# Kernel optimization log

Measured on AMD Instinct MI355X. Metric: run time of the kernel, lower is better.

Reference implementation:

```python
import jax, jax.numpy as jnp
import numpy as np

NC = 2_000_000   # clauses
NV = 500_000     # variables
E = 6_000_000    # edges per polarity


def _inv_sqrt_deg(deg):
    # deg^-0.5 with inf (deg==0) replaced by 0, nan-safe for autodiff
    safe = jnp.where(deg > 0, deg, 1.0)
    return jnp.where(deg > 0, safe ** -0.5, 0.0)


def _conv(x_src, x_trg, inv_src, inv_trg, src, trg, n_trg):
    # G4GCNConv: message = norm * x_j + x_i, aggr='add'
    # (lin_src+relu in the original is dead code: propagate uses raw x)
    norm = inv_src[src] * inv_trg[trg]                     # [E]
    msg = norm[:, None] * x_src[src] + x_trg[trg]          # [E, 2]
    return jax.ops.segment_sum(msg, trg, num_segments=n_trg)  # [n_trg, 2]


def setup_inputs() -> dict:
    key = jax.random.key(0)
    ks = jax.random.split(key, 16)
    inp = {
        'x_clause': jax.random.normal(ks[0], (NC, 1), jnp.float32),
        'x_variable': jax.random.normal(ks[1], (NV, 1), jnp.float32),
        'deg_clause': jax.random.randint(ks[2], (NC,), 0, 16).astype(jnp.float32),
        'deg_variable': jax.random.randint(ks[3], (NV,), 0, 48).astype(jnp.float32),
        'pos_src': jax.random.randint(ks[4], (E,), 0, NC, jnp.int32),
        'pos_trg': jax.random.randint(ks[5], (E,), 0, NV, jnp.int32),
        'neg_src': jax.random.randint(ks[6], (E,), 0, NC, jnp.int32),
        'neg_trg': jax.random.randint(ks[7], (E,), 0, NV, jnp.int32),
        'W0c': jax.random.normal(ks[8], (1, 2), jnp.float32),
        'b0c': jax.random.normal(ks[9], (2,), jnp.float32) * 0.1,
        'W0v': jax.random.normal(ks[10], (1, 2), jnp.float32),
        'b0v': jax.random.normal(ks[11], (2,), jnp.float32) * 0.1,
        'Wc': jax.random.normal(ks[12], (4, 6, 2), jnp.float32) * 0.4,
        'bc': jax.random.normal(ks[13], (4, 2), jnp.float32) * 0.1,
        'Wv': jax.random.normal(ks[14], (4, 6, 2), jnp.float32) * 0.4,
        'bv': jax.random.normal(ks[15], (4, 2), jnp.float32) * 0.1,
    }
    return inp


def reference(x_clause, x_variable, deg_clause, deg_variable,
              pos_src, pos_trg, neg_src, neg_trg,
              W0c, b0c, W0v, b0v, Wc, bc, Wv, bv):
    nc, nv = x_clause.shape[0], x_variable.shape[0]
    inv_c = _inv_sqrt_deg(deg_clause)
    inv_v = _inv_sqrt_deg(deg_variable)

    xc = x_clause @ W0c + b0c    # [NC, 2]
    xv = x_variable @ W0v + b0v  # [NV, 2]

    for l in range(4):
        prev_c, prev_v = xc, xv
        # target 'variable': clause -> variable edges (pos, then neg)
        v_pos = _conv(xc, xv, inv_c, inv_v, pos_src, pos_trg, nv)
        v_neg = _conv(xc, xv, inv_c, inv_v, neg_src, neg_trg, nv)
        # target 'clause': reversed edges, variable -> clause
        c_pos = _conv(xv, xc, inv_v, inv_c, pos_trg, pos_src, nc)
        c_neg = _conv(xv, xc, inv_v, inv_c, neg_trg, neg_src, nc)
        # HeteroConv aggr='cat' then cat with previous state, then 6->2 Linear
        xv = jnp.concatenate([v_pos, v_neg, prev_v], axis=1) @ Wv[l] + bv[l]
        xc = jnp.concatenate([c_pos, c_neg, prev_c], axis=1) @ Wc[l] + bc[l]

    return xv  # [NV, 2]
```

## Files before the change

kernel.cpp:

```cpp
#include <hip/hip_runtime.h>


#define GAB 256
#define BB  1024
#define CAPE 26624

static inline int cdiv_h(long long a, long long b) { return (int)((a + b - 1) / b); }

__device__ inline float bf_lo(unsigned u) { return __uint_as_float(u << 16); }
__device__ inline float bf_hi(unsigned u) { return __uint_as_float(u & 0xffff0000u); }
__device__ inline unsigned packy(float a, float b) {
    unsigned ua = __float_as_uint(a), ub = __float_as_uint(b);
    ua = (ua + 0x7fffu + ((ua >> 16) & 1u)) >> 16;
    ub = (ub + 0x7fffu + ((ub >> 16) & 1u)) & 0xffff0000u;
    return ua | ub;
}


__global__ __launch_bounds__(BB) void hist_both(
    const int* __restrict__ keyV, const int* __restrict__ keyC,
    int e, int chunk, int sv, int sc, int nbv, int nbc,
    unsigned* __restrict__ histV, unsigned* __restrict__ histC) {
    extern __shared__ unsigned h[];
    unsigned* hv = h;
    unsigned* hc = h + nbv * 4;
    int blk = blockIdx.x, tid = threadIdx.x;
    for (int i = tid; i < (nbv + nbc) * 4; i += blockDim.x) h[i] = 0u;
    __syncthreads();
    int s = blk * chunk, epos = min(e, s + chunk);
    int r = tid & 3;
    for (int i = s + tid; i < epos; i += blockDim.x) {
        atomicAdd(&hv[(((unsigned)(keyV[i] >> sv)) << 2) | r], 1u);
        atomicAdd(&hc[(((unsigned)(keyC[i] >> sc)) << 2) | r], 1u);
    }
    __syncthreads();
    for (int i = tid; i < nbv; i += blockDim.x)
        histV[(size_t)i * GAB + blk] = hv[4 * i] + hv[4 * i + 1] + hv[4 * i + 2] + hv[4 * i + 3];
    for (int i = tid; i < nbc; i += blockDim.x)
        histC[(size_t)i * GAB + blk] = hc[4 * i] + hc[4 * i + 1] + hc[4 * i + 2] + hc[4 * i + 3];
}

__global__ void rowscan256(const unsigned* __restrict__ hist, unsigned* __restrict__ rowscan,
                           unsigned* __restrict__ row_total) {
    __shared__ unsigned ts[256];
    int b = blockIdx.x, t = threadIdx.x;
    unsigned v0 = hist[(size_t)b * GAB + t];
    ts[t] = v0;
    __syncthreads();
    for (int off = 1; off < 256; off <<= 1) {
        unsigned v = (t >= off) ? ts[t - off] : 0u;
        __syncthreads();
        ts[t] += v;
        __syncthreads();
    }
    rowscan[(size_t)b * GAB + t] = ts[t] - v0;
    if (t == 255) row_total[b] = ts[255];
}

__global__ void basescan2(const unsigned* __restrict__ totP, const unsigned* __restrict__ totN,
                          unsigned* __restrict__ base, unsigned* __restrict__ baseNeg, int nb) {
    __shared__ unsigned a[2048];
    __shared__ unsigned ts[1024];
    int t = threadIdx.x;
    a[t] = (t < nb) ? (totP[t] + totN[t]) : 0u;
    a[t + 1024] = (t + 1024 < nb) ? (totP[t + 1024] + totN[t + 1024]) : 0u;
    __syncthreads();
    unsigned a0 = a[2 * t], a1 = a[2 * t + 1];
    unsigned sum = a0 + a1;
    ts[t] = sum;
    __syncthreads();
    for (int off = 1; off < 1024; off <<= 1) {
        unsigned v = (t >= off) ? ts[t - off] : 0u;
        __syncthreads();
        ts[t] += v;
        __syncthreads();
    }
    unsigned b0 = ts[t] - sum;
    if (2 * t <= nb) base[2 * t] = b0;
    if (2 * t + 1 <= nb) base[2 * t + 1] = b0 + a0;
    if (2 * t < nb) baseNeg[2 * t] = b0 + totP[2 * t];
    if (2 * t + 1 < nb) baseNeg[2 * t + 1] = b0 + a0 + totP[2 * t + 1];
}

__global__ __launch_bounds__(BB) void scatter_sb(
    const int* __restrict__ key, const int* __restrict__ pay,
    int e, int chunk, int kshift, int nb,
    const unsigned* __restrict__ rowscan, const unsigned* __restrict__ base,
    unsigned* __restrict__ out) {
    extern __shared__ unsigned cur[];
    int blk = blockIdx.x, tid = threadIdx.x;
    for (int i = tid; i < nb; i += blockDim.x)
        cur[i] = base[i] + rowscan[(size_t)i * GAB + blk];
    __syncthreads();
    int s = blk * chunk, epos = min(e, s + chunk);
    unsigned mask = (1u << kshift) - 1u;
    for (int i = s + tid; i < epos; i += blockDim.x) {
        int k = key[i];
        int b = k >> kshift;
        unsigned p = atomicAdd(&cur[b], 1u);
        out[p] = ((unsigned)pay[i] << kshift) | ((unsigned)k & mask);
    }
}

__global__ __launch_bounds__(1024) void localsort_v_m(
    const unsigned* __restrict__ ent, const unsigned* __restrict__ base,
    const unsigned* __restrict__ baseNeg, int nsb, int nv, int cs,
    unsigned* __restrict__ srcs, unsigned* __restrict__ rp, unsigned* __restrict__ cnts) {
    __shared__ unsigned h[4096];
    __shared__ unsigned ts[1024];
    __shared__ unsigned buf[CAPE];
    int s = blockIdx.x, t = threadIdx.x;
    unsigned sb = base[s], pe = baseNeg[s], se = base[s + 1];
    bool fits = (se - sb) <= (unsigned)CAPE;
    for (int k = 0; k < 4; ++k) h[t * 4 + k] = 0u;
    __syncthreads();
    for (unsigned i = sb + t; i < pe; i += 1024) {
        unsigned u = ent[i];
        atomicAdd(&h[((u & 1023u) << 2) | ((u >> 10) >> cs)], 1u);
    }
    __syncthreads();
    unsigned pc[4];
    for (int k = 0; k < 4; ++k) pc[k] = h[t * 4 + k];
    __syncthreads();
    for (unsigned i = pe + t; i < se; i += 1024) {
        unsigned u = ent[i];
        atomicAdd(&h[((u & 1023u) << 2) | ((u >> 10) >> cs)], 1u);
    }
    __syncthreads();
    unsigned v0[4];
    unsigned sum = 0;
    for (int k = 0; k < 4; ++k) { v0[k] = h[t * 4 + k]; sum += v0[k]; }
    ts[t] = sum;
    __syncthreads();
    for (int off = 1; off < 1024; off <<= 1) {
        unsigned x = (t >= off) ? ts[t - off] : 0u;
        __syncthreads();
        ts[t] += x;
        __syncthreads();
    }
    unsigned ex = ts[t] - sum;
    unsigned hx[4];
    for (int k = 0; k < 4; ++k) { hx[k] = ex; ex += v0[k]; }
    int node = s * 1024 + t;
    if (node < nv) {
        for (int ch = 0; ch < 4; ++ch) rp[(size_t)node * 4 + ch] = sb + hx[ch];
        unsigned cp = pc[0] + pc[1] + pc[2] + pc[3];
        unsigned tot = v0[0] + v0[1] + v0[2] + v0[3];
        cnts[node] = (cp << 16) | (tot - cp);
    }
    if (s == nsb - 1 && t == 0) rp[(size_t)nv * 4] = se;
    for (int k = 0; k < 4; ++k) h[t * 4 + k] = hx[k];
    __syncthreads();
    if (fits) {
        for (unsigned i = sb + t; i < pe; i += 1024) {
            unsigned u = ent[i];
            unsigned p = atomicAdd(&h[((u & 1023u) << 2) | ((u >> 10) >> cs)], 1u);
            buf[p] = u >> 10;
        }
        for (unsigned i = pe + t; i < se; i += 1024) {
            unsigned u = ent[i];
            unsigned p = atomicAdd(&h[((u & 1023u) << 2) | ((u >> 10) >> cs)], 1u);
            buf[p] = 0x80000000u | (u >> 10);
        }
        __syncthreads();
        unsigned n = se - sb;
        for (unsigned i = t; i < n; i += 1024) srcs[sb + i] = buf[i];
    } else {
        for (unsigned i = sb + t; i < pe; i += 1024) {
            unsigned u = ent[i];
            unsigned p = atomicAdd(&h[((u & 1023u) << 2) | ((u >> 10) >> cs)], 1u);
            srcs[sb + p] = u >> 10;
        }
        for (unsigned i = pe + t; i < se; i += 1024) {
            unsigned u = ent[i];
            unsigned p = atomicAdd(&h[((u & 1023u) << 2) | ((u >> 10) >> cs)], 1u);
            srcs[sb + p] = 0x80000000u | (u >> 10);
        }
    }
}

__global__ __launch_bounds__(1024) void localsort_c_m(
    const unsigned* __restrict__ ent, const unsigned* __restrict__ base,
    const unsigned* __restrict__ baseNeg, int nsb, int nc,
    unsigned* __restrict__ srcs, unsigned* __restrict__ rp, unsigned* __restrict__ cnts) {
    __shared__ unsigned h[4096];
    __shared__ unsigned ts[1024];
    __shared__ unsigned buf[CAPE];
    int s = blockIdx.x, t = threadIdx.x;
    unsigned sb = base[s], pe = baseNeg[s], se = base[s + 1];
    bool fits = (se - sb) <= (unsigned)CAPE;
    for (int k = 0; k < 4; ++k) h[t * 4 + k] = 0u;
    __syncthreads();
    for (unsigned i = sb + t; i < pe; i += 1024)
        atomicAdd(&h[ent[i] & 4095u], 1u);
    __syncthreads();
    unsigned pc[4];
    for (int k = 0; k < 4; ++k) pc[k] = h[t * 4 + k];
    __syncthreads();
    for (unsigned i = pe + t; i < se; i += 1024)
        atomicAdd(&h[ent[i] & 4095u], 1u);
    __syncthreads();
    unsigned v0[4];
    unsigned sum = 0;
    for (int k = 0; k < 4; ++k) { v0[k] = h[t * 4 + k]; sum += v0[k]; }
    ts[t] = sum;
    __syncthreads();
    for (int off = 1; off < 1024; off <<= 1) {
        unsigned x = (t >= off) ? ts[t - off] : 0u;
        __syncthreads();
        ts[t] += x;
        __syncthreads();
    }
    unsigned ex = ts[t] - sum;
    unsigned hx[4];
    for (int k = 0; k < 4; ++k) { hx[k] = ex; ex += v0[k]; }
    int node0 = s * 4096 + t * 4;
    for (int k = 0; k < 4; ++k) {
        int node = node0 + k;
        if (node < nc) {
            rp[node] = sb + hx[k];
            cnts[node] = (pc[k] << 16) | (v0[k] - pc[k]);
        }
    }
    if (s == nsb - 1 && t == 0) rp[nc] = se;
    for (int k = 0; k < 4; ++k) h[t * 4 + k] = hx[k];
    __syncthreads();
    if (fits) {
        for (unsigned i = sb + t; i < pe; i += 1024) {
            unsigned u = ent[i];
            unsigned p = atomicAdd(&h[u & 4095u], 1u);
            buf[p] = u >> 12;
        }
        for (unsigned i = pe + t; i < se; i += 1024) {
            unsigned u = ent[i];
            unsigned p = atomicAdd(&h[u & 4095u], 1u);
            buf[p] = 0x80000000u | (u >> 12);
        }
        __syncthreads();
        unsigned n = se - sb;
        for (unsigned i = t; i < n; i += 1024) srcs[sb + i] = buf[i];
    } else {
        for (unsigned i = sb + t; i < pe; i += 1024) {
            unsigned u = ent[i];
            unsigned p = atomicAdd(&h[u & 4095u], 1u);
            srcs[sb + p] = u >> 12;
        }
        for (unsigned i = pe + t; i < se; i += 1024) {
            unsigned u = ent[i];
            unsigned p = atomicAdd(&h[u & 4095u], 1u);
            srcs[sb + p] = 0x80000000u | (u >> 12);
        }
    }
}


__global__ void init_c_kernel(const float* __restrict__ x, const float* __restrict__ deg,
                              const float* __restrict__ W0, const float* __restrict__ b0,
                              float2* __restrict__ xc, unsigned* __restrict__ yc, int n) {
    int i = blockIdx.x * blockDim.x + threadIdx.x;
    if (i >= n) return;
    float xi = x[i];
    float2 o = make_float2(fmaf(xi, W0[0], b0[0]), fmaf(xi, W0[1], b0[1]));
    xc[i] = o;
    float d = deg[i];
    float inv = (d > 0.f) ? rsqrtf(d) : 0.f;
    yc[i] = packy(inv * o.x, inv * o.y);
}

__global__ void init_v_kernel(const float* __restrict__ x, const float* __restrict__ deg,
                              const float* __restrict__ W0, const float* __restrict__ b0,
                              float2* __restrict__ xv, unsigned* __restrict__ yv, int n) {
    int i = blockIdx.x * blockDim.x + threadIdx.x;
    if (i >= n) return;
    float xi = x[i];
    float2 o = make_float2(fmaf(xi, W0[0], b0[0]), fmaf(xi, W0[1], b0[1]));
    xv[i] = o;
    float d = deg[i];
    float inv = (d > 0.f) ? rsqrtf(d) : 0.f;
    yv[i] = packy(inv * o.x, inv * o.y);
}


__global__ __launch_bounds__(256) void v_chunk_q(
    const unsigned* __restrict__ rp, const unsigned* __restrict__ srcs,
    const unsigned* __restrict__ yc, float4* __restrict__ acc, int nv, int k) {
    int gt = blockIdx.x * blockDim.x + threadIdx.x;
    int i = gt >> 2, q = gt & 3;
    if (i >= nv) return;
    unsigned s0 = rp[(size_t)i * 4 + k], e0 = rp[(size_t)i * 4 + k + 1];
    float ax = 0.f, ay = 0.f, bx = 0.f, by = 0.f;
    for (unsigned j = s0 + q; j < e0; j += 4) {
        unsigned u = srcs[j];
        unsigned yw = yc[u & 0x7fffffffu];
        float lo = bf_lo(yw), hi = bf_hi(yw);
        float tp = (u & 0x80000000u) ? 0.f : 1.f;
        ax = fmaf(tp, lo, ax); ay = fmaf(tp, hi, ay);
        bx = fmaf(1.f - tp, lo, bx); by = fmaf(1.f - tp, hi, by);
    }
    for (int m = 1; m < 4; m <<= 1) {
        ax += __shfl_xor(ax, m, 4);
        ay += __shfl_xor(ay, m, 4);
        bx += __shfl_xor(bx, m, 4);
        by += __shfl_xor(by, m, 4);
    }
    if (q == 0) {
        float4 a = (k == 0) ? make_float4(0.f, 0.f, 0.f, 0.f) : acc[i];
        a.x += ax; a.y += ay; a.z += bx; a.w += by;
        acc[i] = a;
    }
}

__global__ __launch_bounds__(256) void v_chunk_last(
    const unsigned* __restrict__ rp, const unsigned* __restrict__ srcs,
    const unsigned* __restrict__ yc, const float4* __restrict__ acc,
    const unsigned* __restrict__ cnts, float2* __restrict__ xv,
    const float* __restrict__ deg_v, const float* __restrict__ W,
    const float* __restrict__ bias, unsigned* __restrict__ yv_out, int nv, int writeY) {
    int gt = blockIdx.x * blockDim.x + threadIdx.x;
    int i = gt >> 2, q = gt & 3;
    if (i >= nv) return;
    unsigned s0 = rp[(size_t)i * 4 + 3], e0 = rp[(size_t)i * 4 + 4];
    float ax = 0.f, ay = 0.f, bx = 0.f, by = 0.f;
    for (unsigned j = s0 + q; j < e0; j += 4) {
        unsigned u = srcs[j];
        unsigned yw = yc[u & 0x7fffffffu];
        float lo = bf_lo(yw), hi = bf_hi(yw);
        float tp = (u & 0x80000000u) ? 0.f : 1.f;
        ax = fmaf(tp, lo, ax); ay = fmaf(tp, hi, ay);
        bx = fmaf(1.f - tp, lo, bx); by = fmaf(1.f - tp, hi, by);
    }
    for (int m = 1; m < 4; m <<= 1) {
        ax += __shfl_xor(ax, m, 4);
        ay += __shfl_xor(ay, m, 4);
        bx += __shfl_xor(bx, m, 4);
        by += __shfl_xor(by, m, 4);
    }
    if (q == 0) {
        float4 a = acc[i];
        a.x += ax; a.y += ay; a.z += bx; a.w += by;
        unsigned ct = cnts[i];
        float cp = (float)(ct >> 16), cn = (float)(ct & 0xffffu);
        float2 xi = xv[i];
        float dv = deg_v[i];
        float iv = (dv > 0.f) ? rsqrtf(dv) : 0.f;
        float m0 = fmaf(iv, a.x, cp * xi.x);
        float m1 = fmaf(iv, a.y, cp * xi.y);
        float m2 = fmaf(iv, a.z, cn * xi.x);
        float m3 = fmaf(iv, a.w, cn * xi.y);
        float o0 = bias[0] + m0 * W[0] + m1 * W[2] + m2 * W[4] + m3 * W[6] + xi.x * W[8] + xi.y * W[10];
        float o1 = bias[1] + m0 * W[1] + m1 * W[3] + m2 * W[5] + m3 * W[7] + xi.x * W[9] + xi.y * W[11];
        xv[i] = make_float2(o0, o1);
        if (writeY) yv_out[i] = packy(iv * o0, iv * o1);
    }
}

__global__ __launch_bounds__(256) void c_layer_m(
    const unsigned* __restrict__ rp, const unsigned* __restrict__ srcs,
    const unsigned* __restrict__ cnts, const unsigned* __restrict__ yv,
    float2* __restrict__ xc, const float* __restrict__ deg_c,
    unsigned* __restrict__ yc, const float* __restrict__ W,
    const float* __restrict__ bias, int nc, int writeX) {
    int gt = blockIdx.x * blockDim.x + threadIdx.x;
    int i = gt >> 2, q = gt & 3;
    if (i >= nc) return;
    unsigned s0 = rp[i], e0 = rp[i + 1];
    float ax = 0.f, ay = 0.f, bx = 0.f, by = 0.f;
    for (unsigned j = s0 + q; j < e0; j += 4) {
        unsigned u = srcs[j];
        unsigned yw = yv[u & 0x7fffffffu];
        float lo = bf_lo(yw), hi = bf_hi(yw);
        float tp = (u & 0x80000000u) ? 0.f : 1.f;
        ax = fmaf(tp, lo, ax); ay = fmaf(tp, hi, ay);
        bx = fmaf(1.f - tp, lo, bx); by = fmaf(1.f - tp, hi, by);
    }
    for (int m = 1; m < 4; m <<= 1) {
        ax += __shfl_xor(ax, m, 4);
        ay += __shfl_xor(ay, m, 4);
        bx += __shfl_xor(bx, m, 4);
        by += __shfl_xor(by, m, 4);
    }
    if (q == 0) {
        unsigned ct = cnts[i];
        float cp = (float)(ct >> 16), cn = (float)(ct & 0xffffu);
        float2 xi = xc[i];
        float dc = deg_c[i];
        float ic = (dc > 0.f) ? rsqrtf(dc) : 0.f;
        float m0 = fmaf(ic, ax, cp * xi.x);
        float m1 = fmaf(ic, ay, cp * xi.y);
        float m2 = fmaf(ic, bx, cn * xi.x);
        float m3 = fmaf(ic, by, cn * xi.y);
        float o0 = bias[0] + m0 * W[0] + m1 * W[2] + m2 * W[4] + m3 * W[6] + xi.x * W[8] + xi.y * W[10];
        float o1 = bias[1] + m0 * W[1] + m1 * W[3] + m2 * W[5] + m3 * W[7] + xi.x * W[9] + xi.y * W[11];
        if (writeX) xc[i] = make_float2(o0, o1);
        yc[i] = packy(ic * o0, ic * o1);
    }
}


__global__ void init_nodes(const float* __restrict__ x, const float* __restrict__ deg,
                           const float* __restrict__ W0, const float* __restrict__ b0,
                           float2* __restrict__ xf, float* __restrict__ inv, int n) {
    int i = blockIdx.x * blockDim.x + threadIdx.x;
    if (i >= n) return;
    float xi = x[i];
    xf[i] = make_float2(fmaf(xi, W0[0], b0[0]), fmaf(xi, W0[1], b0[1]));
    float d = deg[i];
    inv[i] = (d > 0.0f) ? (1.0f / sqrtf(d)) : 0.0f;
}

__global__ void count_edges(const int* __restrict__ src, const int* __restrict__ trg,
                            float* __restrict__ cnt_src, float* __restrict__ cnt_trg, int e) {
    int i = blockIdx.x * blockDim.x + threadIdx.x;
    if (i >= e) return;
    atomicAdd(&cnt_src[src[i]], 1.0f);
    atomicAdd(&cnt_trg[trg[i]], 1.0f);
}

__global__ void edge_pass(const int* __restrict__ src, const int* __restrict__ trg,
                          const float2* __restrict__ xc, const float2* __restrict__ xv,
                          const float* __restrict__ inv_c, const float* __restrict__ inv_v,
                          float2* __restrict__ Sv, float2* __restrict__ Sc, int e) {
    int i = blockIdx.x * blockDim.x + threadIdx.x;
    if (i >= e) return;
    int c = src[i];
    int v = trg[i];
    float ic = inv_c[c], iv = inv_v[v];
    float2 a = xc[c];
    float2 b = xv[v];
    atomicAdd(&Sv[v].x, a.x * ic);
    atomicAdd(&Sv[v].y, a.y * ic);
    atomicAdd(&Sc[c].x, b.x * iv);
    atomicAdd(&Sc[c].y, b.y * iv);
}

__global__ void node_update(float2* __restrict__ x, const float2* __restrict__ Sp,
                            const float2* __restrict__ Sn, const float* __restrict__ inv,
                            const float* __restrict__ cp, const float* __restrict__ cn,
                            const float* __restrict__ W, const float* __restrict__ b, int n) {
    int i = blockIdx.x * blockDim.x + threadIdx.x;
    if (i >= n) return;
    float2 xi = x[i];
    float ii = inv[i];
    float2 sp = Sp[i], sn = Sn[i];
    float cpi = cp[i], cni = cn[i];
    float m0 = fmaf(ii, sp.x, cpi * xi.x);
    float m1 = fmaf(ii, sp.y, cpi * xi.y);
    float m2 = fmaf(ii, sn.x, cni * xi.x);
    float m3 = fmaf(ii, sn.y, cni * xi.y);
    float o0 = b[0] + m0 * W[0] + m1 * W[2] + m2 * W[4] + m3 * W[6] + xi.x * W[8] + xi.y * W[10];
    float o1 = b[1] + m0 * W[1] + m1 * W[3] + m2 * W[5] + m3 * W[7] + xi.x * W[9] + xi.y * W[11];
    x[i] = make_float2(o0, o1);
}


extern "C" void kernel_launch(void* const* d_in, const int* in_sizes, int n_in,
                              void* d_out, int out_size, void* d_ws, size_t ws_size,
                              hipStream_t stream) {
    const float* x_clause   = (const float*)d_in[0];
    const float* x_variable = (const float*)d_in[1];
    const float* deg_clause = (const float*)d_in[2];
    const float* deg_var    = (const float*)d_in[3];
    const int*   pos_src    = (const int*)d_in[4];
    const int*   pos_trg    = (const int*)d_in[5];
    const int*   neg_src    = (const int*)d_in[6];
    const int*   neg_trg    = (const int*)d_in[7];
    const float* W0c        = (const float*)d_in[8];
    const float* b0c        = (const float*)d_in[9];
    const float* W0v        = (const float*)d_in[10];
    const float* b0v        = (const float*)d_in[11];
    const float* Wc         = (const float*)d_in[12];
    const float* bc         = (const float*)d_in[13];
    const float* Wv         = (const float*)d_in[14];
    const float* bv         = (const float*)d_in[15];

    const int nc = in_sizes[0];
    const int nv = in_sizes[1];
    const int e  = in_sizes[4];
    const int B = 256;

    const int NSBV = cdiv_h(nv, 1024);
    const int NSBC = cdiv_h(nc, 4096);
    const int maxnb = NSBV > NSBC ? NSBV : NSBC;
    const bool pack_ok = (nc <= (1 << 21)) && (nv <= (1 << 19)) &&
                         (NSBV <= 2040) && (NSBC <= 2040);

    int cs = 0;
    while ((4LL << cs) < nc) cs++;

    {
        size_t off = 0;
        auto alloc = [&](size_t bytes) {
            void* p = (char*)d_ws + off;
            off += (bytes + 255) & ~(size_t)255;
            return p;
        };
        unsigned* srcs_v = (unsigned*)alloc((size_t)2 * e * 4);
        unsigned* srcs_c = (unsigned*)alloc((size_t)2 * e * 4);
        unsigned* rp_v   = (unsigned*)alloc((size_t)4 * (nv + 1) * 4);
        unsigned* rp_c   = (unsigned*)alloc((size_t)(nc + 1) * 4);
        unsigned* cnts_v = (unsigned*)alloc((size_t)nv * 4);
        unsigned* cnts_c = (unsigned*)alloc((size_t)nc * 4);
        const size_t overlay = off;
        unsigned* temp    = (unsigned*)alloc((size_t)2 * e * 4);
        unsigned* histVP  = (unsigned*)alloc((size_t)maxnb * GAB * 4);
        unsigned* histVN  = (unsigned*)alloc((size_t)maxnb * GAB * 4);
        unsigned* histCP  = (unsigned*)alloc((size_t)maxnb * GAB * 4);
        unsigned* histCN  = (unsigned*)alloc((size_t)maxnb * GAB * 4);
        unsigned* rsVP    = (unsigned*)alloc((size_t)maxnb * GAB * 4);
        unsigned* rsVN    = (unsigned*)alloc((size_t)maxnb * GAB * 4);
        unsigned* rsCP    = (unsigned*)alloc((size_t)maxnb * GAB * 4);
        unsigned* rsCN    = (unsigned*)alloc((size_t)maxnb * GAB * 4);
        unsigned* totVP   = (unsigned*)alloc((size_t)maxnb * 4);
        unsigned* totVN   = (unsigned*)alloc((size_t)maxnb * 4);
        unsigned* totCP   = (unsigned*)alloc((size_t)maxnb * 4);
        unsigned* totCN   = (unsigned*)alloc((size_t)maxnb * 4);
        unsigned* baseV   = (unsigned*)alloc((size_t)(NSBV + 1) * 4);
        unsigned* baseVN  = (unsigned*)alloc((size_t)(NSBV + 1) * 4);
        unsigned* baseC   = (unsigned*)alloc((size_t)(NSBC + 1) * 4);
        unsigned* baseCN  = (unsigned*)alloc((size_t)(NSBC + 1) * 4);
        const size_t build_end = off;
        off = overlay;
        float4*   accv    = (float4*)alloc((size_t)nv * 16);
        float2*   xc      = (float2*)alloc((size_t)nc * 8);
        unsigned* yc      = (unsigned*)alloc((size_t)nc * 4);
        unsigned* yvA     = (unsigned*)alloc((size_t)nv * 4);
        unsigned* yvB     = (unsigned*)alloc((size_t)nv * 4);
        const size_t layer_end = off;
        const size_t required = build_end > layer_end ? build_end : layer_end;

        if (required <= ws_size && pack_ok) {
            const int chunk = cdiv_h(e, GAB);
            hist_both<<<GAB, BB, (size_t)(NSBV + NSBC) * 16, stream>>>(
                pos_trg, pos_src, e, chunk, 10, 12, NSBV, NSBC, histVP, histCP);
            hist_both<<<GAB, BB, (size_t)(NSBV + NSBC) * 16, stream>>>(
                neg_trg, neg_src, e, chunk, 10, 12, NSBV, NSBC, histVN, histCN);
            rowscan256<<<NSBV, B, 0, stream>>>(histVP, rsVP, totVP);
            rowscan256<<<NSBV, B, 0, stream>>>(histVN, rsVN, totVN);
            rowscan256<<<NSBC, B, 0, stream>>>(histCP, rsCP, totCP);
            rowscan256<<<NSBC, B, 0, stream>>>(histCN, rsCN, totCN);
            basescan2<<<1, 1024, 0, stream>>>(totVP, totVN, baseV, baseVN, NSBV);
            basescan2<<<1, 1024, 0, stream>>>(totCP, totCN, baseC, baseCN, NSBC);
            scatter_sb<<<GAB, BB, (size_t)NSBV * 4, stream>>>(pos_trg, pos_src, e, chunk,
                                                              10, NSBV, rsVP, baseV, temp);
            scatter_sb<<<GAB, BB, (size_t)NSBV * 4, stream>>>(neg_trg, neg_src, e, chunk,
                                                              10, NSBV, rsVN, baseVN, temp);
            localsort_v_m<<<NSBV, 1024, 0, stream>>>(temp, baseV, baseVN, NSBV, nv, cs,
                                                     srcs_v, rp_v, cnts_v);
            scatter_sb<<<GAB, BB, (size_t)NSBC * 4, stream>>>(pos_src, pos_trg, e, chunk,
                                                              12, NSBC, rsCP, baseC, temp);
            scatter_sb<<<GAB, BB, (size_t)NSBC * 4, stream>>>(neg_src, neg_trg, e, chunk,
                                                              12, NSBC, rsCN, baseCN, temp);
            localsort_c_m<<<NSBC, 1024, 0, stream>>>(temp, baseC, baseCN, NSBC, nc,
                                                     srcs_c, rp_c, cnts_c);

            float2* xv = (float2*)d_out;
            init_c_kernel<<<cdiv_h(nc, B), B, 0, stream>>>(x_clause, deg_clause, W0c, b0c, xc, yc, nc);
            init_v_kernel<<<cdiv_h(nv, B), B, 0, stream>>>(x_variable, deg_var, W0v, b0v, xv, yvA, nv);

            unsigned* ycur = yvA;
            unsigned* ynxt = yvB;
            for (int l = 0; l < 4; ++l) {
                for (int k = 0; k < 3; ++k) {
                    v_chunk_q<<<cdiv_h((long long)nv * 4, B), B, 0, stream>>>(
                        rp_v, srcs_v, yc, accv, nv, k);
                }
                v_chunk_last<<<cdiv_h((long long)nv * 4, B), B, 0, stream>>>(
                    rp_v, srcs_v, yc, accv, cnts_v, xv, deg_var,
                    Wv + l * 12, bv + l * 2, ynxt, nv, (l < 2) ? 1 : 0);
                if (l < 3) {
                    c_layer_m<<<cdiv_h((long long)nc * 4, B), B, 0, stream>>>(
                        rp_c, srcs_c, cnts_c, ycur, xc, deg_clause, yc,
                        Wc + l * 12, bc + l * 2, nc, (l < 2) ? 1 : 0);
                }
                unsigned* ty = ycur; ycur = ynxt; ynxt = ty;
            }
            return;
        }
    }

    char* p = (char*)d_ws;
    float2* Sv_pos = (float2*)p; p += (size_t)nv * sizeof(float2);
    float2* Sv_neg = (float2*)p; p += (size_t)nv * sizeof(float2);
    float2* Sc_pos = (float2*)p; p += (size_t)nc * sizeof(float2);
    float2* Sc_neg = (float2*)p; p += (size_t)nc * sizeof(float2);
    const size_t s_bytes = (size_t)(2 * nv + 2 * nc) * sizeof(float2);
    float2* xc2 = (float2*)p; p += (size_t)nc * sizeof(float2);
    float* inv_c = (float*)p; p += (size_t)nc * sizeof(float);
    float* inv_v = (float*)p; p += (size_t)nv * sizeof(float);
    float* cntc_pos = (float*)p; p += (size_t)nc * sizeof(float);
    float* cntc_neg = (float*)p; p += (size_t)nc * sizeof(float);
    float* cntv_pos = (float*)p; p += (size_t)nv * sizeof(float);
    float* cntv_neg = (float*)p; p += (size_t)nv * sizeof(float);
    const size_t cnt_bytes = (size_t)(2 * nc + 2 * nv) * sizeof(float);
    float2* xv = (float2*)d_out;

    hipMemsetAsync(Sv_pos, 0, s_bytes, stream);
    hipMemsetAsync(cntc_pos, 0, cnt_bytes, stream);
    init_nodes<<<cdiv_h(nc, B), B, 0, stream>>>(x_clause, deg_clause, W0c, b0c, xc2, inv_c, nc);
    init_nodes<<<cdiv_h(nv, B), B, 0, stream>>>(x_variable, deg_var, W0v, b0v, xv, inv_v, nv);
    count_edges<<<cdiv_h(e, B), B, 0, stream>>>(pos_src, pos_trg, cntc_pos, cntv_pos, e);
    count_edges<<<cdiv_h(e, B), B, 0, stream>>>(neg_src, neg_trg, cntc_neg, cntv_neg, e);
    for (int l = 0; l < 4; ++l) {
        edge_pass<<<cdiv_h(e, B), B, 0, stream>>>(pos_src, pos_trg, xc2, xv, inv_c, inv_v,
                                                  Sv_pos, Sc_pos, e);
        edge_pass<<<cdiv_h(e, B), B, 0, stream>>>(neg_src, neg_trg, xc2, xv, inv_c, inv_v,
                                                  Sv_neg, Sc_neg, e);
        node_update<<<cdiv_h(nv, B), B, 0, stream>>>(xv, Sv_pos, Sv_neg, inv_v,
                                                     cntv_pos, cntv_neg, Wv + l * 12, bv + l * 2, nv);
        node_update<<<cdiv_h(nc, B), B, 0, stream>>>(xc2, Sc_pos, Sc_neg, inv_c,
                                                     cntc_pos, cntc_neg, Wc + l * 12, bc + l * 2, nc);
        if (l < 3) hipMemsetAsync(Sv_pos, 0, s_bytes, stream);
    }
}
```

Measured before the change: 998.9 us.

## Fuse chunked variable-side aggregation into one kernel and unroll gather loops by two

Replaces the four per-layer variable-aggregation launches (three chunk kernels plus a finalize kernel) with one kernel that walks all four source chunks per row and applies the linear update directly. This removes the float4 accumulator buffer and its read-modify-write traffic along with three launches per layer. The gather loops in both the variable and clause kernels are also unrolled by two so two independent loads are in flight. The chunking appears to have existed to keep gathers of the clause feature array cache-local per pass, so merging the chunks may reduce cache locality.

```diff
diff --git a/kernel.cpp b/kernel.cpp
--- a/kernel.cpp
+++ b/kernel.cpp
@@ -281,21 +281,43 @@
 }
 
 
-__global__ __launch_bounds__(256) void v_chunk_q(
+__global__ __launch_bounds__(256) void v_layer_k(
     const unsigned* __restrict__ rp, const unsigned* __restrict__ srcs,
-    const unsigned* __restrict__ yc, float4* __restrict__ acc, int nv, int k) {
+    const unsigned* __restrict__ yc, const unsigned* __restrict__ cnts,
+    float2* __restrict__ xv, const float* __restrict__ deg_v,
+    const float* __restrict__ W, const float* __restrict__ bias,
+    unsigned* __restrict__ yv_out, int nv, int writeY) {
     int gt = blockIdx.x * blockDim.x + threadIdx.x;
     int i = gt >> 2, q = gt & 3;
     if (i >= nv) return;
-    unsigned s0 = rp[(size_t)i * 4 + k], e0 = rp[(size_t)i * 4 + k + 1];
+    uint4 rq = *reinterpret_cast<const uint4*>(rp + (size_t)i * 4);
+    unsigned e3 = rp[(size_t)(i + 1) * 4];
     float ax = 0.f, ay = 0.f, bx = 0.f, by = 0.f;
-    for (unsigned j = s0 + q; j < e0; j += 4) {
-        unsigned u = srcs[j];
-        unsigned yw = yc[u & 0x7fffffffu];
-        float lo = bf_lo(yw), hi = bf_hi(yw);
-        float tp = (u & 0x80000000u) ? 0.f : 1.f;
-        ax = fmaf(tp, lo, ax); ay = fmaf(tp, hi, ay);
-        bx = fmaf(1.f - tp, lo, bx); by = fmaf(1.f - tp, hi, by);
+    unsigned segs[5] = { rq.x, rq.y, rq.z, rq.w, e3 };
+    #pragma unroll
+    for (int k = 0; k < 4; ++k) {
+        unsigned s0 = segs[k], e0 = segs[k + 1];
+        unsigned j = s0 + q;
+        for (; j + 4 < e0; j += 8) {
+            unsigned u0 = srcs[j], u1 = srcs[j + 4];
+            unsigned y0 = yc[u0 & 0x7fffffffu], y1 = yc[u1 & 0x7fffffffu];
+            float t0 = (u0 & 0x80000000u) ? 0.f : 1.f;
+            float t1 = (u1 & 0x80000000u) ? 0.f : 1.f;
+            float l0 = bf_lo(y0), h0 = bf_hi(y0);
+            float l1 = bf_lo(y1), h1 = bf_hi(y1);
+            ax = fmaf(t0, l0, ax); ay = fmaf(t0, h0, ay);
+            bx = fmaf(1.f - t0, l0, bx); by = fmaf(1.f - t0, h0, by);
+            ax = fmaf(t1, l1, ax); ay = fmaf(t1, h1, ay);
+            bx = fmaf(1.f - t1, l1, bx); by = fmaf(1.f - t1, h1, by);
+        }
+        if (j < e0) {
+            unsigned u = srcs[j];
+            unsigned yw = yc[u & 0x7fffffffu];
+            float tp = (u & 0x80000000u) ? 0.f : 1.f;
+            float lo = bf_lo(yw), hi = bf_hi(yw);
+            ax = fmaf(tp, lo, ax); ay = fmaf(tp, hi, ay);
+            bx = fmaf(1.f - tp, lo, bx); by = fmaf(1.f - tp, hi, by);
+        }
     }
     for (int m = 1; m < 4; m <<= 1) {
         ax += __shfl_xor(ax, m, 4);
@@ -304,49 +326,15 @@
         by += __shfl_xor(by, m, 4);
     }
     if (q == 0) {
-        float4 a = (k == 0) ? make_float4(0.f, 0.f, 0.f, 0.f) : acc[i];
-        a.x += ax; a.y += ay; a.z += bx; a.w += by;
-        acc[i] = a;
-    }
-}
-
-__global__ __launch_bounds__(256) void v_chunk_last(
-    const unsigned* __restrict__ rp, const unsigned* __restrict__ srcs,
-    const unsigned* __restrict__ yc, const float4* __restrict__ acc,
-    const unsigned* __restrict__ cnts, float2* __restrict__ xv,
-    const float* __restrict__ deg_v, const float* __restrict__ W,
-    const float* __restrict__ bias, unsigned* __restrict__ yv_out, int nv, int writeY) {
-    int gt = blockIdx.x * blockDim.x + threadIdx.x;
-    int i = gt >> 2, q = gt & 3;
-    if (i >= nv) return;
-    unsigned s0 = rp[(size_t)i * 4 + 3], e0 = rp[(size_t)i * 4 + 4];
-    float ax = 0.f, ay = 0.f, bx = 0.f, by = 0.f;
-    for (unsigned j = s0 + q; j < e0; j += 4) {
-        unsigned u = srcs[j];
-        unsigned yw = yc[u & 0x7fffffffu];
-        float lo = bf_lo(yw), hi = bf_hi(yw);
-        float tp = (u & 0x80000000u) ? 0.f : 1.f;
-        ax = fmaf(tp, lo, ax); ay = fmaf(tp, hi, ay);
-        bx = fmaf(1.f - tp, lo, bx); by = fmaf(1.f - tp, hi, by);
-    }
-    for (int m = 1; m < 4; m <<= 1) {
-        ax += __shfl_xor(ax, m, 4);
-        ay += __shfl_xor(ay, m, 4);
-        bx += __shfl_xor(bx, m, 4);
-        by += __shfl_xor(by, m, 4);
-    }
-    if (q == 0) {
-        float4 a = acc[i];
-        a.x += ax; a.y += ay; a.z += bx; a.w += by;
         unsigned ct = cnts[i];
         float cp = (float)(ct >> 16), cn = (float)(ct & 0xffffu);
         float2 xi = xv[i];
         float dv = deg_v[i];
         float iv = (dv > 0.f) ? rsqrtf(dv) : 0.f;
-        float m0 = fmaf(iv, a.x, cp * xi.x);
-        float m1 = fmaf(iv, a.y, cp * xi.y);
-        float m2 = fmaf(iv, a.z, cn * xi.x);
-        float m3 = fmaf(iv, a.w, cn * xi.y);
+        float m0 = fmaf(iv, ax, cp * xi.x);
+        float m1 = fmaf(iv, ay, cp * xi.y);
+        float m2 = fmaf(iv, bx, cn * xi.x);
+        float m3 = fmaf(iv, by, cn * xi.y);
         float o0 = bias[0] + m0 * W[0] + m1 * W[2] + m2 * W[4] + m3 * W[6] + xi.x * W[8] + xi.y * W[10];
         float o1 = bias[1] + m0 * W[1] + m1 * W[3] + m2 * W[5] + m3 * W[7] + xi.x * W[9] + xi.y * W[11];
         xv[i] = make_float2(o0, o1);
@@ -365,11 +353,24 @@
     if (i >= nc) return;
     unsigned s0 = rp[i], e0 = rp[i + 1];
     float ax = 0.f, ay = 0.f, bx = 0.f, by = 0.f;
-    for (unsigned j = s0 + q; j < e0; j += 4) {
+    unsigned j = s0 + q;
+    for (; j + 4 < e0; j += 8) {
+        unsigned u0 = srcs[j], u1 = srcs[j + 4];
+        unsigned y0 = yv[u0 & 0x7fffffffu], y1 = yv[u1 & 0x7fffffffu];
+        float t0 = (u0 & 0x80000000u) ? 0.f : 1.f;
+        float t1 = (u1 & 0x80000000u) ? 0.f : 1.f;
+        float l0 = bf_lo(y0), h0 = bf_hi(y0);
+        float l1 = bf_lo(y1), h1 = bf_hi(y1);
+        ax = fmaf(t0, l0, ax); ay = fmaf(t0, h0, ay);
+        bx = fmaf(1.f - t0, l0, bx); by = fmaf(1.f - t0, h0, by);
+        ax = fmaf(t1, l1, ax); ay = fmaf(t1, h1, ay);
+        bx = fmaf(1.f - t1, l1, bx); by = fmaf(1.f - t1, h1, by);
+    }
+    if (j < e0) {
         unsigned u = srcs[j];
         unsigned yw = yv[u & 0x7fffffffu];
+        float tp = (u & 0x80000000u) ? 0.f : 1.f;
         float lo = bf_lo(yw), hi = bf_hi(yw);
-        float tp = (u & 0x80000000u) ? 0.f : 1.f;
         ax = fmaf(tp, lo, ax); ay = fmaf(tp, hi, ay);
         bx = fmaf(1.f - tp, lo, bx); by = fmaf(1.f - tp, hi, by);
     }
@@ -520,7 +521,6 @@
         unsigned* baseCN  = (unsigned*)alloc((size_t)(NSBC + 1) * 4);
         const size_t build_end = off;
         off = overlay;
-        float4*   accv    = (float4*)alloc((size_t)nv * 16);
         float2*   xc      = (float2*)alloc((size_t)nc * 8);
         unsigned* yc      = (unsigned*)alloc((size_t)nc * 4);
         unsigned* yvA     = (unsigned*)alloc((size_t)nv * 4);
@@ -560,12 +560,8 @@
             unsigned* ycur = yvA;
             unsigned* ynxt = yvB;
             for (int l = 0; l < 4; ++l) {
-                for (int k = 0; k < 3; ++k) {
-                    v_chunk_q<<<cdiv_h((long long)nv * 4, B), B, 0, stream>>>(
-                        rp_v, srcs_v, yc, accv, nv, k);
-                }
-                v_chunk_last<<<cdiv_h((long long)nv * 4, B), B, 0, stream>>>(
-                    rp_v, srcs_v, yc, accv, cnts_v, xv, deg_var,
+                v_layer_k<<<cdiv_h((long long)nv * 4, B), B, 0, stream>>>(
+                    rp_v, srcs_v, yc, cnts_v, xv, deg_var,
                     Wv + l * 12, bv + l * 2, ynxt, nv, (l < 2) ? 1 : 0);
                 if (l < 3) {
                     c_layer_m<<<cdiv_h((long long)nc * 4, B), B, 0, stream>>>(
```

Result: slower. 1.110 ms (+11.1%).
